# Optimization experiments

Hardware: AMD Instinct MI355X
Metric: run time of the kernel (lower is better)

The kernel has to match this reference:

```python
import jax, jax.numpy as jnp
import numpy as np
import math

NN_K = 32          # num_neighbor = ceil(k/dilation) = 32
MAP_SIZE = 32
GROUP = 4


def _fibonacci_sphere(samples):
    # matches fibonacci_sphere(samples, randomize=False): rnd = 1.0
    pts = [[0.0, 0.0, 0.0]]
    offset = 2.0 / samples
    increment = math.pi * (3.0 - math.sqrt(5.0))
    for i in range(samples - 1):
        y = i * offset - 1 + offset / 2.0
        r = math.sqrt(1.0 - y * y)
        phi = ((i + 1.0) % samples) * increment
        pts.append([math.cos(phi) * r, y, math.sin(phi) * r])
    return np.asarray(pts, dtype=np.float32)


def setup_inputs() -> dict:
    B, N, C_in, C_out = 8, 2048, 64, 128
    key = jax.random.key(0)
    ks = jax.random.split(key, 6)
    x = jax.random.normal(ks[0], (B, 3, N), dtype=jnp.float32)
    feature = jax.random.normal(ks[1], (B, C_in, N), dtype=jnp.float32)
    neigh_indexs = jax.random.randint(ks[2], (B, N, NN_K), 0, N, dtype=jnp.int32)
    B_rff = jax.random.normal(ks[3], (7, MAP_SIZE), dtype=jnp.float32)  # frozen RFF proj
    kernels = jnp.asarray(_fibonacci_sphere(NN_K).T)                    # [3, NN_K], frozen
    mlp_w = jax.random.normal(ks[4], (C_in, 2 * MAP_SIZE), dtype=jnp.float32) * 0.05
    mlp_b = jnp.zeros((C_in,), dtype=jnp.float32)
    conv_w = jax.random.normal(ks[5], (C_out, 2 * C_in * NN_K), dtype=jnp.float32) * 0.02
    conv_b = jnp.zeros((C_out,), dtype=jnp.float32)
    return {"x": x, "feature": feature, "neigh_indexs": neigh_indexs,
            "B_rff": B_rff, "kernels": kernels,
            "mlp_w": mlp_w, "mlp_b": mlp_b, "conv_w": conv_w, "conv_b": conv_b}


def _topkmax(perm):
    # two normalization passes over axis=1 (rows), squaring in between, then hard threshold
    perm = perm / (jnp.sum(perm, axis=1, keepdims=True) + 1e-6)
    perm = perm * perm
    perm = perm / (jnp.sum(perm, axis=1, keepdims=True) + 1e-6)
    return jnp.where(perm > 0.1, perm, 0.0)


def _paiconv(x, feature, neigh_indexs, B_rff, kernels, mlp_w, mlp_b, conv_w, conv_b):
    bsz, C, N = feature.shape           # B, num_feat, num_pts
    nn_k = neigh_indexs.shape[-1]
    xp = jnp.transpose(x, (0, 2, 1))    # [B, N, 3]

    # neighbor gather of coordinates -> [B*N, nn, 3]
    x_neighs = jax.vmap(lambda p, i: p[i])(xp, neigh_indexs).reshape(bsz * N, nn_k, 3)
    x_rep = jnp.broadcast_to(x_neighs[:, :1, :], x_neighs.shape)
    x_rel = x_neighs - x_rep
    x_dis = jnp.linalg.norm(x_rel, axis=-1, keepdims=True)

    # random Fourier features + 1x1 conv (mlp)
    pos = (2.0 * math.pi) * jnp.concatenate([x_rep, x_rel, x_dis], axis=-1)  # [BN, nn, 7]
    xf = pos @ B_rff                                                          # [BN, nn, 32]
    xf = jnp.concatenate([jnp.sin(xf), jnp.cos(xf)], axis=-1)                 # [BN, nn, 64]
    xf = jnp.einsum('oc,bnc->bon', mlp_w, xf) + mlp_b[None, :, None]          # [BN, C, nn]

    # neighbor gather of features -> [BN, C, nn], concat with positional feats
    fp = jnp.transpose(feature, (0, 2, 1))                                    # [B, N, C]
    f_nb = jax.vmap(lambda p, i: p[i])(fp, neigh_indexs).reshape(bsz * N, nn_k, C)
    feats = jnp.concatenate([jnp.transpose(f_nb, (0, 2, 1)), xf], axis=1)     # [BN, 2C, nn]

    # permutation/attention matrix
    one_pad = jnp.zeros((nn_k, nn_k), dtype=x.dtype).at[0, 0].set(1.0)
    perm = x_rel @ kernels + one_pad                                          # [BN, nn, nn]
    perm = jnp.where(perm > 0, perm, 0.0)
    perm = _topkmax(perm)

    if C > 3:  # static channel shuffle with group=4
        feats = feats.reshape(bsz * N, GROUP, 2 * C // GROUP, nn_k)
        feats = jnp.transpose(feats, (0, 2, 1, 3)).reshape(bsz * N, 2 * C, nn_k)

    feats = feats @ perm                                                      # [BN, 2C, nn]
    feats = feats.reshape(bsz * N, 2 * C * nn_k)
    out = feats @ conv_w.T + conv_b                                           # [BN, out_c]
    return jnp.transpose(out.reshape(bsz, N, -1), (0, 2, 1))                  # [B, out_c, N]


def reference(x, feature, neigh_indexs, B_rff, kernels, mlp_w, mlp_b, conv_w, conv_b):
    return _paiconv(x, feature, neigh_indexs, B_rff, kernels, mlp_w, mlp_b, conv_w, conv_b)
```

## Files before the change

kernel.cpp:

```cpp
#include <hip/hip_runtime.h>
#include <hip/hip_bf16.h>

typedef unsigned short ushort_t;
typedef __attribute__((ext_vector_type(8))) short short8;
typedef __attribute__((ext_vector_type(4))) float floatx4;

#define TWO_PI 6.28318530717958647692f

__device__ __forceinline__ float bf2f(ushort_t u) {
  union { unsigned u; float f; } v; v.u = ((unsigned)u) << 16; return v.f;
}
__device__ __forceinline__ unsigned pk(float a, float b) {
  union { __hip_bfloat162 h2; unsigned u; } v;
  v.h2 = __float22bfloat162_rn(make_float2(a, b));
  return v.u;
}
__device__ __forceinline__ float ldin(const void* p, int idx, bool bf) {
  return bf ? bf2f(((const ushort_t*)p)[idx]) : ((const float*)p)[idx];
}
__device__ __forceinline__ bool detect_bf16(const void* xv) {
  const ushort_t* us = (const ushort_t*)xv;
  unsigned u = us[threadIdx.x & 63];
  int e = (u >> 7) & 0xFF;
  bool good = (e >= 110) && (e <= 133);
  unsigned long long m = __ballot(good);
  return __builtin_popcountll(m) >= 52;
}
__device__ __forceinline__ uint4 pack8f(const float* p) {
  float4 a = *(const float4*)p, b = *(const float4*)(p + 4);
  uint4 r;
  r.x = pk(a.x, a.y); r.y = pk(a.z, a.w);
  r.z = pk(b.x, b.y); r.w = pk(b.z, b.w);
  return r;
}

__device__ __forceinline__ void gload16(const void* g, void* l) {
  __builtin_amdgcn_global_load_lds(
      (const __attribute__((address_space(1))) unsigned*)g,
      (__attribute__((address_space(3))) unsigned*)l, 16, 0, 0);
}

__global__ __launch_bounds__(256) void paiconv_prep(
    const void* __restrict__ xprobe, const void* __restrict__ feat,
    ushort_t* __restrict__ Ft, const void* __restrict__ W,
    ushort_t* __restrict__ Wc)
{
  const bool bfm = detect_bf16(xprobe);
  const int t = threadIdx.x;
  __shared__ ushort_t tile[64 * 72];

  if (blockIdx.x >= 256) {
    int i = ((blockIdx.x - 256) * 256 + t) << 3;
    int n = i >> 12, rem = i & 4095;
    int c = rem >> 5, j = rem & 31;
    int src = (n << 12) + (((c & 31) * 4 + (c >> 5)) << 5) + j;
    if (bfm) *(uint4*)(Wc + i) = *(const uint4*)((const ushort_t*)W + src);
    else     *(uint4*)(Wc + i) = pack8f((const float*)W + src);
    return;
  }

  const int bb = blockIdx.x >> 5;
  const int n0 = (blockIdx.x & 31) << 6;
  {
    const int c = t & 63, ng = t >> 6;
    size_t base = (((size_t)(bb * 64 + c)) << 11) + n0 + (ng << 4);
    ushort_t v[16];
    if (bfm) {
      const ushort_t* fp_ = (const ushort_t*)feat + base;
      uint4 a = *(const uint4*)fp_, b2 = *(const uint4*)(fp_ + 8);
      unsigned uu[8] = {a.x, a.y, a.z, a.w, b2.x, b2.y, b2.z, b2.w};
#pragma unroll
      for (int e = 0; e < 8; ++e) {
        v[2 * e] = (ushort_t)(uu[e] & 0xffff);
        v[2 * e + 1] = (ushort_t)(uu[e] >> 16);
      }
    } else {
      const float* fp_ = (const float*)feat + base;
#pragma unroll
      for (int k = 0; k < 16; k += 2) {
        unsigned u = pk(fp_[k], fp_[k + 1]);
        v[k] = (ushort_t)(u & 0xffff);
        v[k + 1] = (ushort_t)(u >> 16);
      }
    }
#pragma unroll
    for (int k = 0; k < 16; ++k) tile[(ng * 16 + k) * 72 + c] = v[k];
  }
  __syncthreads();
  {
    const int nn = t >> 2, qtr = t & 3;
    uint4 w0 = *(const uint4*)(tile + nn * 72 + qtr * 16);
    uint4 w1 = *(const uint4*)(tile + nn * 72 + qtr * 16 + 8);
    ushort_t* dst = Ft + (((size_t)(bb * 2048 + n0 + nn)) << 6) + (qtr << 4);
    *(uint4*)dst = w0;
    *(uint4*)(dst + 8) = w1;
  }
}

#define SFPT 5184
__global__ __launch_bounds__(256) void paiconv_phase1(
    const void* __restrict__ x,
    const ushort_t* __restrict__ Ft,
    const int*  __restrict__ nbr,
    const void* __restrict__ Brff,
    const void* __restrict__ kern,
    const void* __restrict__ mlpw,
    const void* __restrict__ mlpb,
    ushort_t*   __restrict__ Ag)
{
  const bool bfm = detect_bf16(x);
  const int t = threadIdx.x;
  const int p0 = blockIdx.x << 1;
  const int b  = p0 >> 11;
  const int w = t >> 6, lane = t & 63, lrow = lane & 15, quad = lane >> 4;

  __shared__ ushort_t sRt[64 * 72];
  __shared__ ushort_t sF[SFPT];
  __shared__ ushort_t sP[2 * 32 * 40];
  __shared__ float sRel[2][32][3];
  __shared__ float sDis[2][32];
  __shared__ float sRep[2][3];
  __shared__ float sBr[224];

  const int gpt = t >> 7, gj = (t >> 2) & 31, gch = t & 3;
  const int gidx = nbr[((p0 + gpt) << 5) + gj];
  const ushort_t* gfr = Ft + (((size_t)(b * 2048 + gidx)) << 6) + (gch << 4);
  uint4 g0 = ((const uint4*)gfr)[0];
  uint4 g1 = ((const uint4*)gfr)[1];

  const int pj = t & 31;
  const float kn0 = ldin(kern, pj, bfm);
  const float kn1 = ldin(kern, 32 + pj, bfm);
  const float kn2 = ldin(kern, 64 + pj, bfm);
  const int mc = (w << 4) + lrow;
  const float bv = ldin(mlpb, mc, bfm);

  short8 mb0, mb1;
  if (bfm) {
    const ushort_t* mp = (const ushort_t*)mlpw + mc * 64;
    mb0 = *(const short8*)(mp + (quad << 3));
    mb1 = *(const short8*)(mp + 32 + (quad << 3));
  } else {
    const float* mp = (const float*)mlpw + mc * 64;
    uint4 u0 = pack8f(mp + (quad << 3));
    uint4 u1 = pack8f(mp + 32 + (quad << 3));
    mb0 = *(short8*)&u0;
    mb1 = *(short8*)&u1;
  }

  if (t < 224) sBr[t] = ldin(Brff, t, bfm);
  if (t < 64) {
    int pt = t >> 5, i = t & 31;
    int p = p0 + pt;
    int idx  = nbr[(p << 5) + i];
    int idx0 = nbr[(p << 5)];
    int xo = b * 6144;
    float rx = ldin(x, xo + idx0, bfm);
    float ry = ldin(x, xo + 2048 + idx0, bfm);
    float rz = ldin(x, xo + 4096 + idx0, bfm);
    float cx = ldin(x, xo + idx, bfm);
    float cy = ldin(x, xo + 2048 + idx, bfm);
    float cz = ldin(x, xo + 4096 + idx, bfm);
    float dx = cx - rx, dy = cy - ry, dz = cz - rz;
    sRel[pt][i][0] = dx; sRel[pt][i][1] = dy; sRel[pt][i][2] = dz;
    sDis[pt][i] = sqrtf(dx * dx + dy * dy + dz * dz);
    if (i == 0) { sRep[pt][0] = rx; sRep[pt][1] = ry; sRep[pt][2] = rz; }
  }
  __syncthreads();

  {
    int jn = t >> 2, mh = (t & 3) << 3;
    int pt = jn >> 5, j = jn & 31;
    float pos[7];
    pos[0] = TWO_PI * sRep[pt][0]; pos[1] = TWO_PI * sRep[pt][1];
    pos[2] = TWO_PI * sRep[pt][2];
    pos[3] = TWO_PI * sRel[pt][j][0]; pos[4] = TWO_PI * sRel[pt][j][1];
    pos[5] = TWO_PI * sRel[pt][j][2];
    pos[6] = TWO_PI * sDis[pt][j];
    unsigned sw[4], cw[4];
#pragma unroll
    for (int mm = 0; mm < 8; mm += 2) {
      float a0 = 0.f, a1 = 0.f;
#pragma unroll
      for (int d = 0; d < 7; ++d) {
        a0 += pos[d] * sBr[d * 32 + mh + mm];
        a1 += pos[d] * sBr[d * 32 + mh + mm + 1];
      }
      sw[mm >> 1] = pk(__sinf(a0), __sinf(a1));
      cw[mm >> 1] = pk(__cosf(a0), __cosf(a1));
    }
    ushort_t* rb = sRt + jn * 72;
    *(uint4*)(rb + mh)      = make_uint4(sw[0], sw[1], sw[2], sw[3]);
    *(uint4*)(rb + 32 + mh) = make_uint4(cw[0], cw[1], cw[2], cw[3]);
  }
  if (t < 128) {
    int pt = t >> 6, h = (t >> 5) & 1;
    float col[16];
    float s1 = 0.f;
#pragma unroll
    for (int il = 0; il < 16; ++il) {
      int i = h * 16 + il;
      float v = sRel[pt][i][0] * kn0 + sRel[pt][i][1] * kn1 + sRel[pt][i][2] * kn2;
      if (i == 0 && pj == 0) v += 1.0f;
      v = fmaxf(v, 0.f);
      col[il] = v; s1 += v;
    }
    s1 += __shfl_xor(s1, 32, 64);
    float inv1 = 1.0f / (s1 + 1e-6f);
    float s2 = 0.f;
#pragma unroll
    for (int il = 0; il < 16; ++il) { float v = col[il] * inv1; v = v * v; col[il] = v; s2 += v; }
    s2 += __shfl_xor(s2, 32, 64);
    float inv2 = 1.0f / (s2 + 1e-6f);
    unsigned pw[8];
#pragma unroll
    for (int il = 0; il < 16; il += 2) {
      float v0 = col[il] * inv2;     v0 = (v0 > 0.1f) ? v0 : 0.f;
      float v1 = col[il + 1] * inv2; v1 = (v1 > 0.1f) ? v1 : 0.f;
      pw[il >> 1] = pk(v0, v1);
    }
    ushort_t* dst = sP + pt * 1280 + pj * 40 + h * 16;
    *(uint4*)dst       = make_uint4(pw[0], pw[1], pw[2], pw[3]);
    *(uint4*)(dst + 8) = make_uint4(pw[4], pw[5], pw[6], pw[7]);
  }
  __syncthreads();

  const int rbase = (64 + mc) * 40 + ((4 + w) << 3);

#pragma unroll
  for (int pt = 0; pt < 2; ++pt) {
    {
#pragma unroll
      for (int half = 0; half < 2; ++half) {
        int mt = pt * 2 + half;
        const ushort_t* rp = sRt + (mt * 16 + lrow) * 72 + (quad << 3);
        short8 a0 = *(const short8*)rp;
        short8 a1 = *(const short8*)(rp + 32);
        floatx4 acc = {0.f, 0.f, 0.f, 0.f};
        acc = __builtin_amdgcn_mfma_f32_16x16x32_bf16(a0, mb0, acc, 0, 0, 0);
        acc = __builtin_amdgcn_mfma_f32_16x16x32_bf16(a1, mb1, acc, 0, 0, 0);
        int j0 = (half << 4) + (quad << 2);
        *(uint2*)(sF + rbase + j0) =
            make_uint2(pk(acc[0] + bv, acc[1] + bv), pk(acc[2] + bv, acc[3] + bv));
      }
      if (gpt == pt) {
        ushort_t* fp_ = sF + gch * 648 + gj;
        unsigned uu[8] = {g0.x, g0.y, g0.z, g0.w, g1.x, g1.y, g1.z, g1.w};
#pragma unroll
        for (int u = 0; u < 8; ++u) {
          fp_[(2 * u) * 40]     = (ushort_t)(uu[u] & 0xffff);
          fp_[(2 * u + 1) * 40] = (ushort_t)(uu[u] >> 16);
        }
      }
    }
    __syncthreads();

    {
      const ushort_t* Pp = sP + pt * 1280;
      short8 a0 = *(const short8*)(Pp + lrow * 40 + (quad << 3));
      short8 a1 = *(const short8*)(Pp + (16 + lrow) * 40 + (quad << 3));
      size_t prow = ((size_t)(p0 + pt)) << 12;
#pragma unroll
      for (int nt = 0; nt < 2; ++nt) {
        int blk = w * 2 + nt;
        int cidx = (blk << 4) + lrow;
        short8 bfg = *(const short8*)(sF + cidx * 40 + (blk << 3) + (quad << 3));
        floatx4 z = {0.f, 0.f, 0.f, 0.f};
        floatx4 c0 = __builtin_amdgcn_mfma_f32_16x16x32_bf16(a0, bfg, z, 0, 0, 0);
        floatx4 c1 = __builtin_amdgcn_mfma_f32_16x16x32_bf16(a1, bfg, z, 0, 0, 0);
        ushort_t* ad = Ag + prow + cidx * 32 + (quad << 2);
        *(uint2*)ad        = make_uint2(pk(c0[0], c0[1]), pk(c0[2], c0[3]));
        *(uint2*)(ad + 16) = make_uint2(pk(c1[0], c1[1]), pk(c1[2], c1[3]));
      }
    }
    if (pt == 0) __syncthreads();
  }
}

__global__ __launch_bounds__(512) void paiconv_gemm(
    const ushort_t* __restrict__ A,
    const ushort_t* __restrict__ Wc,
    float* __restrict__ part)
{
  __shared__ ushort_t lAs[3 * 64 * 64];
  __shared__ ushort_t lBs[3 * 128 * 64];
  const int m0 = blockIdx.x << 6;
  const int K0 = blockIdx.y << 11;
  const int t = threadIdx.x;
  const int w = t >> 6, lane = t & 63;
  const int wm = w & 1, wn = w >> 1, lrow = lane & 15, quad = lane >> 4;
  const int sx = lrow & 7;

  const int srow = t >> 3, schk = t & 7;
  const int gchk = schk ^ (srow & 7);
  const ushort_t* Agp  = A  + (size_t)(m0 + srow) * 4096 + K0 + (gchk << 3);
  const ushort_t* Bgp0 = Wc + (size_t)srow * 4096        + K0 + (gchk << 3);
  const ushort_t* Bgp1 = Wc + (size_t)(64 + srow) * 4096 + K0 + (gchk << 3);
  const int wb = w << 9;

  floatx4 acc[2][2];
#pragma unroll
  for (int i = 0; i < 2; ++i)
#pragma unroll
    for (int j = 0; j < 2; ++j) acc[i][j] = (floatx4){0.f, 0.f, 0.f, 0.f};

#define STAGE(buf, kbn) do { int off_ = (kbn) << 6;                          \
    gload16(Agp  + off_, lAs + (buf) * 4096 + wb);                           \
    gload16(Bgp0 + off_, lBs + (buf) * 8192 + wb);                           \
    gload16(Bgp1 + off_, lBs + (buf) * 8192 + 4096 + wb); } while (0)

#define COMPUTE(buf) do {                                                    \
    const ushort_t* la_ = lAs + (buf) * 4096;                                \
    const ushort_t* lb_ = lBs + (buf) * 8192;                                \
    _Pragma("unroll")                                                        \
    for (int kk = 0; kk < 2; ++kk) {                                         \
      int ch = ((((kk << 2) + quad) ^ sx) << 3);                             \
      short8 af0 = *(const short8*)(la_ + (((wm << 5) + lrow) << 6) + ch);   \
      short8 af1 = *(const short8*)(la_ + (((wm << 5) + 16 + lrow) << 6) + ch); \
      _Pragma("unroll")                                                      \
      for (int ni = 0; ni < 2; ++ni) {                                       \
        short8 bf = *(const short8*)(lb_ + (((wn << 5) + (ni << 4) + lrow) << 6) + ch); \
        acc[0][ni] = __builtin_amdgcn_mfma_f32_16x16x32_bf16(af0, bf, acc[0][ni], 0, 0, 0); \
        acc[1][ni] = __builtin_amdgcn_mfma_f32_16x16x32_bf16(af1, bf, acc[1][ni], 0, 0, 0); \
      } } } while (0)

#define VMW(n) asm volatile("s_waitcnt vmcnt(" #n ")" ::: "memory")
#define BAR() __builtin_amdgcn_s_barrier()
#define SB0() __builtin_amdgcn_sched_barrier(0)

  STAGE(0, 0);
  STAGE(1, 1);

  for (int g = 0; g < 10; ++g) {
    const int kb = g * 3;
    STAGE(2, kb + 2); VMW(6); BAR(); SB0(); COMPUTE(0); BAR();
    STAGE(0, kb + 3); VMW(6); BAR(); SB0(); COMPUTE(1); BAR();
    STAGE(1, kb + 4); VMW(6); BAR(); SB0(); COMPUTE(2); BAR();
  }
  VMW(3); BAR(); SB0(); COMPUTE(0);
  VMW(0); BAR(); SB0(); COMPUTE(1);

#undef STAGE
#undef COMPUTE
#undef VMW
#undef BAR
#undef SB0

  float* dst = part + ((size_t)blockIdx.y << 21);
#pragma unroll
  for (int mi = 0; mi < 2; ++mi)
#pragma unroll
    for (int ni = 0; ni < 2; ++ni)
#pragma unroll
      for (int r = 0; r < 4; ++r) {
        int m = m0 + (wm << 5) + (mi << 4) + (quad << 2) + r;
        int n = (wn << 5) + (ni << 4) + lrow;
        dst[(size_t)m * 128 + n] = acc[mi][ni][r];
      }
}

__global__ __launch_bounds__(256) void paiconv_reduce(
    const void* __restrict__ xprobe, const float* __restrict__ part,
    const void* __restrict__ bias, void* __restrict__ out)
{
  const bool bfm = detect_bf16(xprobe);
  __shared__ float buf[128 * 65];
  const int m0 = blockIdx.x << 6;
  const int b = m0 >> 11, n0 = m0 & 2047;
  const int t = threadIdx.x;

#pragma unroll
  for (int i = 0; i < 8; ++i) {
    int idx = (i * 256 + t) << 2;
    int mt = idx >> 7, c = idx & 127;
    size_t o = (size_t)(m0 + mt) * 128 + c;
    float4 v0 = *(const float4*)(part + o);
    float4 v1 = *(const float4*)(part + (1u << 21) + o);
    buf[(c + 0) * 65 + mt] = v0.x + v1.x + ldin(bias, c + 0, bfm);
    buf[(c + 1) * 65 + mt] = v0.y + v1.y + ldin(bias, c + 1, bfm);
    buf[(c + 2) * 65 + mt] = v0.z + v1.z + ldin(bias, c + 2, bfm);
    buf[(c + 3) * 65 + mt] = v0.w + v1.w + ldin(bias, c + 3, bfm);
  }
  __syncthreads();
#pragma unroll
  for (int i = 0; i < 8; ++i) {
    int idx = (i * 256 + t) << 2;
    int c = idx >> 6, nl = idx & 63;
    float v0 = buf[c * 65 + nl], v1 = buf[c * 65 + nl + 1];
    float v2 = buf[c * 65 + nl + 2], v3 = buf[c * 65 + nl + 3];
    size_t o = (size_t)b * 262144 + (size_t)c * 2048 + n0 + nl;
    if (bfm) *(uint2*)((ushort_t*)out + o) = make_uint2(pk(v0, v1), pk(v2, v3));
    else     *(float4*)((float*)out + o) = make_float4(v0, v1, v2, v3);
  }
}

extern "C" void kernel_launch(void* const* d_in, const int* in_sizes, int n_in,
                              void* d_out, int out_size, void* d_ws, size_t ws_size,
                              hipStream_t stream) {
  const void* x     = d_in[0];
  const void* feat  = d_in[1];
  const int*  nbr   = (const int*)d_in[2];
  const void* Brff  = d_in[3];
  const void* kern  = d_in[4];
  const void* mlpw  = d_in[5];
  const void* mlpb  = d_in[6];
  const void* convw = d_in[7];
  const void* convb = d_in[8];

  char* ws = (char*)d_ws;
  ushort_t* A   = (ushort_t*)ws;
  ushort_t* Wcv = (ushort_t*)(ws + (size_t)134217728);
  float*    prt = (float*)(ws + (size_t)135266304);
  ushort_t* Ft  = (ushort_t*)(ws + (size_t)152043520);

  paiconv_prep<<<512, 256, 0, stream>>>(x, feat, Ft, convw, Wcv);
  paiconv_phase1<<<8192, 256, 0, stream>>>(x, Ft, nbr, Brff, kern, mlpw, mlpb, A);
  paiconv_gemm<<<dim3(256, 2, 1), 512, 0, stream>>>(A, Wcv, prt);
  paiconv_reduce<<<256, 256, 0, stream>>>(x, prt, convb, d_out);
}
```

Before: 162.3 us.

## Drop split-K in final GEMM and fuse bias/transpose epilogue into it

The GEMM no longer splits K across two blocks. Each of 256 blocks now runs the full K=4096 loop, then transposes its tile through shared memory, adds bias and writes the output directly. This removes the separate reduce kernel, one launch, and the round trip of the fp32 partial buffers through memory. In exchange the grid halves to 256 blocks, which lowers parallelism on a GPU with many CUs and doubles the serial K loop per block.

```diff
diff --git a/kernel.cpp b/kernel.cpp
--- a/kernel.cpp
+++ b/kernel.cpp
@@ -278,14 +278,17 @@
 }
 
 __global__ __launch_bounds__(512) void paiconv_gemm(
+    const void* __restrict__ xprobe,
     const ushort_t* __restrict__ A,
     const ushort_t* __restrict__ Wc,
-    float* __restrict__ part)
+    const void* __restrict__ bias,
+    void* __restrict__ out)
 {
-  __shared__ ushort_t lAs[3 * 64 * 64];
-  __shared__ ushort_t lBs[3 * 128 * 64];
+  const bool bfm = detect_bf16(xprobe);
+  __shared__ ushort_t lsm[3 * 64 * 64 + 3 * 128 * 64];
+  ushort_t* lAs = lsm;
+  ushort_t* lBs = lsm + 3 * 4096;
   const int m0 = blockIdx.x << 6;
-  const int K0 = blockIdx.y << 11;
   const int t = threadIdx.x;
   const int w = t >> 6, lane = t & 63;
   const int wm = w & 1, wn = w >> 1, lrow = lane & 15, quad = lane >> 4;
@@ -293,9 +296,9 @@
 
   const int srow = t >> 3, schk = t & 7;
   const int gchk = schk ^ (srow & 7);
-  const ushort_t* Agp  = A  + (size_t)(m0 + srow) * 4096 + K0 + (gchk << 3);
-  const ushort_t* Bgp0 = Wc + (size_t)srow * 4096        + K0 + (gchk << 3);
-  const ushort_t* Bgp1 = Wc + (size_t)(64 + srow) * 4096 + K0 + (gchk << 3);
+  const ushort_t* Agp  = A  + (size_t)(m0 + srow) * 4096 + (gchk << 3);
+  const ushort_t* Bgp0 = Wc + (size_t)srow * 4096        + (gchk << 3);
+  const ushort_t* Bgp1 = Wc + (size_t)(64 + srow) * 4096 + (gchk << 3);
   const int wb = w << 9;
 
   floatx4 acc[2][2];
@@ -331,14 +334,16 @@
   STAGE(0, 0);
   STAGE(1, 1);
 
-  for (int g = 0; g < 10; ++g) {
+  for (int g = 0; g < 20; ++g) {
     const int kb = g * 3;
     STAGE(2, kb + 2); VMW(6); BAR(); SB0(); COMPUTE(0); BAR();
     STAGE(0, kb + 3); VMW(6); BAR(); SB0(); COMPUTE(1); BAR();
     STAGE(1, kb + 4); VMW(6); BAR(); SB0(); COMPUTE(2); BAR();
   }
-  VMW(3); BAR(); SB0(); COMPUTE(0);
-  VMW(0); BAR(); SB0(); COMPUTE(1);
+  STAGE(2, 62); VMW(6); BAR(); SB0(); COMPUTE(0); BAR();
+  STAGE(0, 63); VMW(6); BAR(); SB0(); COMPUTE(1); BAR();
+  VMW(3); BAR(); SB0(); COMPUTE(2);
+  VMW(0); BAR(); SB0(); COMPUTE(0);
 
 #undef STAGE
 #undef COMPUTE
@@ -346,51 +351,30 @@
 #undef BAR
 #undef SB0
 
-  float* dst = part + ((size_t)blockIdx.y << 21);
+  __syncthreads();
+  float* buf = (float*)lsm;
+  const int b = m0 >> 11, n0 = m0 & 2047;
 #pragma unroll
   for (int mi = 0; mi < 2; ++mi)
 #pragma unroll
     for (int ni = 0; ni < 2; ++ni)
 #pragma unroll
       for (int r = 0; r < 4; ++r) {
-        int m = m0 + (wm << 5) + (mi << 4) + (quad << 2) + r;
+        int m = (wm << 5) + (mi << 4) + (quad << 2) + r;
         int n = (wn << 5) + (ni << 4) + lrow;
-        dst[(size_t)m * 128 + n] = acc[mi][ni][r];
-      }
-}
-
-__global__ __launch_bounds__(256) void paiconv_reduce(
-    const void* __restrict__ xprobe, const float* __restrict__ part,
-    const void* __restrict__ bias, void* __restrict__ out)
-{
-  const bool bfm = detect_bf16(xprobe);
-  __shared__ float buf[128 * 65];
-  const int m0 = blockIdx.x << 6;
-  const int b = m0 >> 11, n0 = m0 & 2047;
-  const int t = threadIdx.x;
-
-#pragma unroll
-  for (int i = 0; i < 8; ++i) {
-    int idx = (i * 256 + t) << 2;
-    int mt = idx >> 7, c = idx & 127;
-    size_t o = (size_t)(m0 + mt) * 128 + c;
-    float4 v0 = *(const float4*)(part + o);
-    float4 v1 = *(const float4*)(part + (1u << 21) + o);
-    buf[(c + 0) * 65 + mt] = v0.x + v1.x + ldin(bias, c + 0, bfm);
-    buf[(c + 1) * 65 + mt] = v0.y + v1.y + ldin(bias, c + 1, bfm);
-    buf[(c + 2) * 65 + mt] = v0.z + v1.z + ldin(bias, c + 2, bfm);
-    buf[(c + 3) * 65 + mt] = v0.w + v1.w + ldin(bias, c + 3, bfm);
-  }
+        buf[n * 65 + m] = acc[mi][ni][r];
+      }
   __syncthreads();
 #pragma unroll
-  for (int i = 0; i < 8; ++i) {
-    int idx = (i * 256 + t) << 2;
-    int c = idx >> 6, nl = idx & 63;
-    float v0 = buf[c * 65 + nl], v1 = buf[c * 65 + nl + 1];
-    float v2 = buf[c * 65 + nl + 2], v3 = buf[c * 65 + nl + 3];
-    size_t o = (size_t)b * 262144 + (size_t)c * 2048 + n0 + nl;
+  for (int i = 0; i < 4; ++i) {
+    int lin = (i << 9) + t;
+    int chn = lin >> 4, nl = (lin & 15) << 2;
+    float vb = ldin(bias, chn, bfm);
+    float v0 = buf[chn * 65 + nl + 0] + vb, v1 = buf[chn * 65 + nl + 1] + vb;
+    float v2 = buf[chn * 65 + nl + 2] + vb, v3 = buf[chn * 65 + nl + 3] + vb;
+    size_t o = (size_t)b * 262144 + (size_t)chn * 2048 + n0 + nl;
     if (bfm) *(uint2*)((ushort_t*)out + o) = make_uint2(pk(v0, v1), pk(v2, v3));
-    else     *(float4*)((float*)out + o) = make_float4(v0, v1, v2, v3);
+    else     *(float4*)((float*)out + o)   = make_float4(v0, v1, v2, v3);
   }
 }
 
@@ -410,11 +394,9 @@
   char* ws = (char*)d_ws;
   ushort_t* A   = (ushort_t*)ws;
   ushort_t* Wcv = (ushort_t*)(ws + (size_t)134217728);
-  float*    prt = (float*)(ws + (size_t)135266304);
   ushort_t* Ft  = (ushort_t*)(ws + (size_t)152043520);
 
   paiconv_prep<<<512, 256, 0, stream>>>(x, feat, Ft, convw, Wcv);
   paiconv_phase1<<<8192, 256, 0, stream>>>(x, Ft, nbr, Brff, kern, mlpw, mlpb, A);
-  paiconv_gemm<<<dim3(256, 2, 1), 512, 0, stream>>>(A, Wcv, prt);
-  paiconv_reduce<<<256, 256, 0, stream>>>(x, prt, convb, d_out);
-}
+  paiconv_gemm<<<256, 512, 0, stream>>>(x, A, Wcv, convb, d_out);
+}
```

Measured after the change: 149.8 us, median of 3. 1.08x faster.
